# Optimization experiments

Measured on AMD Instinct MI355X. Metric: run time of the kernel, lower is better.

The kernel has to match this reference:

```python
import jax, jax.numpy as jnp
import numpy as np

N = 6144
IN_DIM = 256
HID = 64
HEADS = 4
LAT = 32
ALPHA = 0.2  # LeakyReLU negative slope
NEG_INF = -9e15


def setup_inputs() -> dict:
    key = jax.random.key(0)
    ks = jax.random.split(key, 6)
    x = jax.random.normal(ks[0], (N, IN_DIM), jnp.float32)
    # sparse symmetric 0/1 adjacency, avg degree ~ 25
    A = (jax.random.uniform(ks[1], (N, N)) < 0.004).astype(jnp.float32)
    A = jnp.maximum(A, A.T)
    # xavier-uniform-ish params, matching pyGAT GraphAttentionLayer shapes
    s1 = float(np.sqrt(6.0 / (IN_DIM + HID)))
    W_heads = jax.random.uniform(ks[2], (HEADS, IN_DIM, HID), jnp.float32, -s1, s1)
    sa = float(np.sqrt(6.0 / (2 * HID + 1)))
    a_heads = jax.random.uniform(ks[3], (HEADS, 2 * HID), jnp.float32, -sa, sa)
    s2 = float(np.sqrt(6.0 / (HEADS * HID + LAT)))
    W_out = jax.random.uniform(ks[4], (HEADS * HID, LAT), jnp.float32, -s2, s2)
    sb = float(np.sqrt(6.0 / (2 * LAT + 1)))
    a_out = jax.random.uniform(ks[5], (2 * LAT,), jnp.float32, -sb, sb)
    return {"x": x, "A": A, "W_heads": W_heads, "a_heads": a_heads,
            "W_out": W_out, "a_out": a_out}


def _gat_layer(h, adj_mask, W, a, concat):
    # h: [N, F_in], W: [F_in, F], a: [2F]
    Wh = h @ W                              # [N, F]
    f = W.shape[1]
    e_src = Wh @ a[:f]                      # [N]
    e_dst = Wh @ a[f:]                      # [N]
    e = jax.nn.leaky_relu(e_src[:, None] + e_dst[None, :], ALPHA)  # [N, N]
    e = jnp.where(adj_mask, e, NEG_INF)
    att = jax.nn.softmax(e, axis=1)         # masked softmax over neighbors
    out = att @ Wh                          # [N, F]
    return jax.nn.elu(out) if concat else out


def reference(x, A, W_heads, a_heads, W_out, a_out):
    # normalize(A, 'sym', False): D^{-1/2} A D^{-1/2}
    deg = A.sum(axis=1)
    dinv = jnp.where(deg > 0, deg ** -0.5, 0.0)
    An = A * dinv[:, None] * dinv[None, :]
    mask = An > 0
    heads = [_gat_layer(x, mask, W_heads[i], a_heads[i], True) for i in range(HEADS)]
    h = jnp.concatenate(heads, axis=1)      # [N, HEADS*HID]
    z = jax.nn.elu(_gat_layer(h, mask, W_out, a_out, False))  # [N, LAT]
    return jax.nn.sigmoid(z @ z.T)          # [N, N]
```

## Files before the change

kernel.cpp:

```cpp
#include <hip/hip_runtime.h>
#include <hip/hip_bf16.h>

#define NN 6144
#define IN_DIM 256
#define HID 64
#define HEADS 4
#define LAT 32
#define CAP 192
#define ALPHA 0.2f
#define GEMM_BLOCKS 384

typedef __attribute__((ext_vector_type(8))) short bf16x8;
typedef __attribute__((ext_vector_type(4))) float f32x4;

__device__ __forceinline__ float elu_f(float v)   { return v > 0.f ? v : expm1f(v); }
__device__ __forceinline__ float lrelu_f(float v) { return v > 0.f ? v : ALPHA * v; }

__device__ __forceinline__ void split_bf16(float v, unsigned short& hi, unsigned short& lo) {
    unsigned u = __builtin_bit_cast(unsigned, v);
    hi = (unsigned short)(u >> 16);
    float vh = __builtin_bit_cast(float, u & 0xFFFF0000u);
    float rl = v - vh;
    lo = (unsigned short)(__builtin_bit_cast(unsigned, rl) >> 16);
}

__global__ __launch_bounds__(256) void k_pre(const float* __restrict__ A,
                                             const float* __restrict__ x,
                                             const float* __restrict__ Wheads,
                                             const float* __restrict__ aheads,
                                             int* __restrict__ nbr, int* __restrict__ cnt,
                                             float* __restrict__ Wh,
                                             float* __restrict__ es, float* __restrict__ ed) {
    __shared__ __align__(16) float smem[2048];
    int bid = blockIdx.x;
    int t = threadIdx.x;
    if (bid < GEMM_BLOCKS) {
        int head = bid & 3, m0 = (bid >> 2) * 64;
        float (*As)[64] = (float(*)[64])smem;
        float (*Bs)[64] = (float(*)[64])(smem + 1024);
        const float* Wc = Wheads + (size_t)head * IN_DIM * HID;
        int ty = t >> 4, tx = t & 15;
        float acc[4][4] = {};
        for (int k0 = 0; k0 < IN_DIM; k0 += 16) {
            {
                int row = t >> 2, k4 = (t & 3) * 4;
                float4 v = *(const float4*)(x + (size_t)(m0 + row) * IN_DIM + k0 + k4);
                As[k4 + 0][row] = v.x; As[k4 + 1][row] = v.y;
                As[k4 + 2][row] = v.z; As[k4 + 3][row] = v.w;
                int kk = t >> 4, n4 = (t & 15) * 4;
                *(float4*)&Bs[kk][n4] = *(const float4*)(Wc + (size_t)(k0 + kk) * HID + n4);
            }
            __syncthreads();
            #pragma unroll
            for (int k = 0; k < 16; ++k) {
                float4 av = *(float4*)&As[k][ty * 4];
                float4 bv = *(float4*)&Bs[k][tx * 4];
                float ar[4] = {av.x, av.y, av.z, av.w};
                float br[4] = {bv.x, bv.y, bv.z, bv.w};
                #pragma unroll
                for (int i = 0; i < 4; ++i)
                    #pragma unroll
                    for (int j = 0; j < 4; ++j)
                        acc[i][j] = fmaf(ar[i], br[j], acc[i][j]);
            }
            __syncthreads();
        }
        #pragma unroll
        for (int i = 0; i < 4; ++i) {
            float4 o = make_float4(acc[i][0], acc[i][1], acc[i][2], acc[i][3]);
            *(float4*)(Wh + (size_t)(m0 + ty * 4 + i) * (HEADS * HID) + head * HID + tx * 4) = o;
        }
        float4 a1v = *(const float4*)(aheads + head * 2 * HID + tx * 4);
        float4 a2v = *(const float4*)(aheads + head * 2 * HID + HID + tx * 4);
        #pragma unroll
        for (int i = 0; i < 4; ++i) {
            float p1 = acc[i][0] * a1v.x + acc[i][1] * a1v.y + acc[i][2] * a1v.z + acc[i][3] * a1v.w;
            float p2 = acc[i][0] * a2v.x + acc[i][1] * a2v.y + acc[i][2] * a2v.z + acc[i][3] * a2v.w;
            #pragma unroll
            for (int off = 8; off; off >>= 1) {
                p1 += __shfl_down(p1, off, 16);
                p2 += __shfl_down(p2, off, 16);
            }
            if (tx == 0) {
                es[head * NN + m0 + ty * 4 + i] = p1;
                ed[head * NN + m0 + ty * 4 + i] = p2;
            }
        }
    } else {
        int row = bid - GEMM_BLOCKS;
        int* lcnt = (int*)smem;
        const float4* Arow = (const float4*)(A + (size_t)row * NN);
        if (t == 0) *lcnt = 0;
        __syncthreads();
        int* my = nbr + (size_t)row * CAP;
        #pragma unroll
        for (int it = 0; it < NN / 4 / 256; ++it) {
            int idx4 = it * 256 + t;
            float4 v = Arow[idx4];
            int base = idx4 * 4;
            if (v.x != 0.f) { int p = atomicAdd(lcnt, 1); if (p < CAP) my[p] = base; }
            if (v.y != 0.f) { int p = atomicAdd(lcnt, 1); if (p < CAP) my[p] = base + 1; }
            if (v.z != 0.f) { int p = atomicAdd(lcnt, 1); if (p < CAP) my[p] = base + 2; }
            if (v.w != 0.f) { int p = atomicAdd(lcnt, 1); if (p < CAP) my[p] = base + 3; }
        }
        __syncthreads();
        if (t == 0) cnt[row] = *lcnt < CAP ? *lcnt : CAP;
    }
}

__global__ __launch_bounds__(256, 8) void k_attn1g2(const int* __restrict__ nbr, const int* __restrict__ cnt,
                                                    const float* __restrict__ es, const float* __restrict__ ed,
                                                    const float* __restrict__ Wh,
                                                    const float* __restrict__ Wout, const float* __restrict__ aout,
                                                    float* __restrict__ Wh2,
                                                    float* __restrict__ es2, float* __restrict__ ed2) {
    __shared__ int col[CAP];
    __shared__ float att[HEADS][CAP];
    __shared__ float hrow[HEADS * HID];
    __shared__ float part[8][LAT];
    int i = blockIdx.x;
    int t = threadIdx.x, h = t >> 6, l = t & 63;
    int c = cnt[i];
    float hval;
    if (c == 0) {
        float s = 0.f;
        for (int r = 0; r < NN; ++r) s += Wh[(size_t)r * (HEADS * HID) + h * HID + l];
        hval = elu_f(s * (1.0f / NN));
    } else {
        const int* nb = nbr + (size_t)i * CAP;
        float esi = es[h * NN + i];
        float m = -3.0e38f;
        for (int j = l; j < c; j += 64) {
            int cj = nb[j];
            if (h == 0) col[j] = cj;
            float e = lrelu_f(esi + ed[h * NN + cj]);
            att[h][j] = e;
            m = fmaxf(m, e);
        }
        #pragma unroll
        for (int off = 32; off; off >>= 1) m = fmaxf(m, __shfl_down(m, off));
        m = __shfl(m, 0);
        float s = 0.f;
        for (int j = l; j < c; j += 64) {
            float p = __expf(att[h][j] - m);
            att[h][j] = p;
            s += p;
        }
        #pragma unroll
        for (int off = 32; off; off >>= 1) s += __shfl_down(s, off);
        s = __shfl(s, 0);
        __syncthreads();
        float inv = 1.0f / s;
        const float* WhH = Wh + h * HID + l;
        float a0 = 0.f, a1 = 0.f, a2 = 0.f, a3 = 0.f;
        float a4 = 0.f, a5 = 0.f, a6 = 0.f, a7 = 0.f;
        int j = 0;
        for (; j + 8 <= c; j += 8) {
            a0 = fmaf(att[h][j + 0], WhH[(size_t)col[j + 0] * (HEADS * HID)], a0);
            a1 = fmaf(att[h][j + 1], WhH[(size_t)col[j + 1] * (HEADS * HID)], a1);
            a2 = fmaf(att[h][j + 2], WhH[(size_t)col[j + 2] * (HEADS * HID)], a2);
            a3 = fmaf(att[h][j + 3], WhH[(size_t)col[j + 3] * (HEADS * HID)], a3);
            a4 = fmaf(att[h][j + 4], WhH[(size_t)col[j + 4] * (HEADS * HID)], a4);
            a5 = fmaf(att[h][j + 5], WhH[(size_t)col[j + 5] * (HEADS * HID)], a5);
            a6 = fmaf(att[h][j + 6], WhH[(size_t)col[j + 6] * (HEADS * HID)], a6);
            a7 = fmaf(att[h][j + 7], WhH[(size_t)col[j + 7] * (HEADS * HID)], a7);
        }
        for (; j < c; ++j)
            a0 = fmaf(att[h][j], WhH[(size_t)col[j] * (HEADS * HID)], a0);
        hval = elu_f((((a0 + a1) + (a2 + a3)) + ((a4 + a5) + (a6 + a7))) * inv);
    }
    hrow[h * HID + l] = hval;
    __syncthreads();
    {
        int half = l >> 5, cc = l & 31;
        int tbase = h * HID + half * 32;
        float p = 0.f;
        #pragma unroll 8
        for (int tt = 0; tt < 32; ++tt)
            p = fmaf(hrow[tbase + tt], Wout[(tbase + tt) * LAT + cc], p);
        part[h * 2 + half][cc] = p;
    }
    __syncthreads();
    if (t < 32) {
        float acc = 0.f;
        #pragma unroll
        for (int w = 0; w < 8; ++w) acc += part[w][t];
        Wh2[(size_t)i * LAT + t] = acc;
        float p1 = acc * aout[t], p2 = acc * aout[LAT + t];
        #pragma unroll
        for (int off = 16; off; off >>= 1) {
            p1 += __shfl_down(p1, off, 32);
            p2 += __shfl_down(p2, off, 32);
        }
        if (t == 0) { es2[i] = p1; ed2[i] = p2; }
    }
}

__global__ __launch_bounds__(256, 8) void k_attn2(const int* __restrict__ nbr, const int* __restrict__ cnt,
                                                  const float* __restrict__ es2, const float* __restrict__ ed2,
                                                  const float* __restrict__ Wh2,
                                                  unsigned short* __restrict__ zh, unsigned short* __restrict__ zl) {
    __shared__ float att[4][CAP];
    __shared__ int col[4][CAP];
    int w = threadIdx.x >> 6, l = threadIdx.x & 63;
    int i = blockIdx.x * 4 + w;
    int c = cnt[i];
    if (c == 0) {
        if (l < LAT) {
            float s = 0.f;
            for (int r = 0; r < NN; ++r) s += Wh2[(size_t)r * LAT + l];
            unsigned short hi, lo;
            split_bf16(elu_f(s * (1.0f / NN)), hi, lo);
            zh[(size_t)i * LAT + l] = hi;
            zl[(size_t)i * LAT + l] = lo;
        }
        return;
    }
    float esi = es2[i];
    const int* nb = nbr + (size_t)i * CAP;
    float m = -3.0e38f;
    for (int j = l; j < c; j += 64) {
        int cj = nb[j];
        col[w][j] = cj;
        float e = lrelu_f(esi + ed2[cj]);
        att[w][j] = e;
        m = fmaxf(m, e);
    }
    #pragma unroll
    for (int off = 32; off; off >>= 1) m = fmaxf(m, __shfl_down(m, off));
    m = __shfl(m, 0);
    float s = 0.f;
    for (int j = l; j < c; j += 64) {
        float p = __expf(att[w][j] - m);
        att[w][j] = p;
        s += p;
    }
    #pragma unroll
    for (int off = 32; off; off >>= 1) s += __shfl_down(s, off);
    s = __shfl(s, 0);
    if (l < LAT) {
        float inv = 1.0f / s;
        float a0 = 0.f, a1 = 0.f, a2 = 0.f, a3 = 0.f;
        int j = 0;
        for (; j + 4 <= c; j += 4) {
            a0 = fmaf(att[w][j + 0], Wh2[(size_t)col[w][j + 0] * LAT + l], a0);
            a1 = fmaf(att[w][j + 1], Wh2[(size_t)col[w][j + 1] * LAT + l], a1);
            a2 = fmaf(att[w][j + 2], Wh2[(size_t)col[w][j + 2] * LAT + l], a2);
            a3 = fmaf(att[w][j + 3], Wh2[(size_t)col[w][j + 3] * LAT + l], a3);
        }
        for (; j < c; ++j)
            a0 = fmaf(att[w][j], Wh2[(size_t)col[w][j] * LAT + l], a0);
        unsigned short hi, lo;
        split_bf16(elu_f(((a0 + a1) + (a2 + a3)) * inv), hi, lo);
        zh[(size_t)i * LAT + l] = hi;
        zl[(size_t)i * LAT + l] = lo;
    }
}

__global__ __launch_bounds__(256, 8) void k_zzt(const unsigned short* __restrict__ zh,
                                                const unsigned short* __restrict__ zl,
                                                float* __restrict__ out) {
    int t = threadIdx.x, w = t >> 6, l = t & 63;
    int m0 = blockIdx.y * 64 + w * 16;
    int n0 = blockIdx.x * 64;
    int r = l & 15, kg = (l >> 4) * 8;
    bf16x8 ah = *(const bf16x8*)(zh + (size_t)(m0 + r) * LAT + kg);
    bf16x8 al = *(const bf16x8*)(zl + (size_t)(m0 + r) * LAT + kg);
    #pragma unroll
    for (int jp = 0; jp < 2; ++jp) {
        int nbA = n0 + (jp * 2 + 0) * 16;
        int nbB = n0 + (jp * 2 + 1) * 16;
        bf16x8 bhA = *(const bf16x8*)(zh + (size_t)(nbA + r) * LAT + kg);
        bf16x8 blA = *(const bf16x8*)(zl + (size_t)(nbA + r) * LAT + kg);
        bf16x8 bhB = *(const bf16x8*)(zh + (size_t)(nbB + r) * LAT + kg);
        bf16x8 blB = *(const bf16x8*)(zl + (size_t)(nbB + r) * LAT + kg);
        f32x4 accA = {0.f, 0.f, 0.f, 0.f};
        accA = __builtin_amdgcn_mfma_f32_16x16x32_bf16(ah, bhA, accA, 0, 0, 0);
        accA = __builtin_amdgcn_mfma_f32_16x16x32_bf16(ah, blA, accA, 0, 0, 0);
        accA = __builtin_amdgcn_mfma_f32_16x16x32_bf16(al, bhA, accA, 0, 0, 0);
        f32x4 accB = {0.f, 0.f, 0.f, 0.f};
        accB = __builtin_amdgcn_mfma_f32_16x16x32_bf16(ah, bhB, accB, 0, 0, 0);
        accB = __builtin_amdgcn_mfma_f32_16x16x32_bf16(ah, blB, accB, 0, 0, 0);
        accB = __builtin_amdgcn_mfma_f32_16x16x32_bf16(al, bhB, accB, 0, 0, 0);
        #pragma unroll
        for (int rr = 0; rr < 4; ++rr) {
            int row = m0 + (l >> 4) * 4 + rr;
            out[(size_t)row * NN + nbA + (l & 15)] = 1.0f / (1.0f + __expf(-accA[rr]));
            out[(size_t)row * NN + nbB + (l & 15)] = 1.0f / (1.0f + __expf(-accB[rr]));
        }
    }
}

extern "C" void kernel_launch(void* const* d_in, const int* in_sizes, int n_in,
                              void* d_out, int out_size, void* d_ws, size_t ws_size,
                              hipStream_t stream) {
    const float* x      = (const float*)d_in[0];
    const float* A      = (const float*)d_in[1];
    const float* Wheads = (const float*)d_in[2];
    const float* aheads = (const float*)d_in[3];
    const float* Wout   = (const float*)d_in[4];
    const float* aout   = (const float*)d_in[5];
    float* out = (float*)d_out;

    char* ws = (char*)d_ws;
    size_t o = 0;
    auto alloc = [&](size_t bytes) { void* p = ws + o; o += (bytes + 255) & ~(size_t)255; return p; };
    int*   nbr   = (int*)  alloc((size_t)NN * CAP * 4);
    int*   cnt   = (int*)  alloc((size_t)NN * 4);
    float* Wh    = (float*)alloc((size_t)NN * HEADS * HID * 4);
    float* es    = (float*)alloc((size_t)HEADS * NN * 4);
    float* ed    = (float*)alloc((size_t)HEADS * NN * 4);
    float* Wh2   = (float*)alloc((size_t)NN * LAT * 4);
    float* es2   = (float*)alloc((size_t)NN * 4);
    float* ed2   = (float*)alloc((size_t)NN * 4);
    unsigned short* zh = (unsigned short*)alloc((size_t)NN * LAT * 2);
    unsigned short* zl = (unsigned short*)alloc((size_t)NN * LAT * 2);

    k_pre     <<<GEMM_BLOCKS + NN, 256, 0, stream>>>(A, x, Wheads, aheads, nbr, cnt, Wh, es, ed);
    k_attn1g2 <<<NN, 256, 0, stream>>>(nbr, cnt, es, ed, Wh, Wout, aout, Wh2, es2, ed2);
    k_attn2   <<<NN / 4, 256, 0, stream>>>(nbr, cnt, es2, ed2, Wh2, zh, zl);
    k_zzt     <<<dim3(NN / 64, NN / 64), 256, 0, stream>>>(zh, zl, out);
}
```

Measured before the change: 115.6 us.

## Fuse adjacency scan into attention kernel and vectorize sigmoid output stores

Splits the former combined GEMM+adjacency-scan kernel into a standalone GEMM, and moves the per-row adjacency scan into the first attention kernel, which builds neighbor lists directly in shared memory and skips re-reading them from global memory. It also changes the ZZ^T output write to store float4s along the transposed index, relying on symmetry of the output. This is meant to cut a global round trip for neighbor lists and make output stores wider. The trade-off is that the attention kernel now serializes the dense A row scan before compute.

```diff
diff --git a/kernel.cpp b/kernel.cpp
--- a/kernel.cpp
+++ b/kernel.cpp
@@ -8,7 +8,6 @@
 #define LAT 32
 #define CAP 192
 #define ALPHA 0.2f
-#define GEMM_BLOCKS 384
 
 typedef __attribute__((ext_vector_type(8))) short bf16x8;
 typedef __attribute__((ext_vector_type(4))) float f32x4;
@@ -24,116 +23,108 @@
     lo = (unsigned short)(__builtin_bit_cast(unsigned, rl) >> 16);
 }
 
-__global__ __launch_bounds__(256) void k_pre(const float* __restrict__ A,
-                                             const float* __restrict__ x,
-                                             const float* __restrict__ Wheads,
-                                             const float* __restrict__ aheads,
-                                             int* __restrict__ nbr, int* __restrict__ cnt,
-                                             float* __restrict__ Wh,
-                                             float* __restrict__ es, float* __restrict__ ed) {
-    __shared__ __align__(16) float smem[2048];
-    int bid = blockIdx.x;
+__global__ __launch_bounds__(256) void k_gemm1(const float* __restrict__ x,
+                                               const float* __restrict__ Wheads,
+                                               const float* __restrict__ aheads,
+                                               float* __restrict__ Wh,
+                                               float* __restrict__ es, float* __restrict__ ed) {
+    __shared__ float As[16][64];
+    __shared__ float Bs[16][64];
+    int head = blockIdx.x & 3, m0 = (blockIdx.x >> 2) * 64;
+    const float* Wc = Wheads + (size_t)head * IN_DIM * HID;
     int t = threadIdx.x;
-    if (bid < GEMM_BLOCKS) {
-        int head = bid & 3, m0 = (bid >> 2) * 64;
-        float (*As)[64] = (float(*)[64])smem;
-        float (*Bs)[64] = (float(*)[64])(smem + 1024);
-        const float* Wc = Wheads + (size_t)head * IN_DIM * HID;
-        int ty = t >> 4, tx = t & 15;
-        float acc[4][4] = {};
-        for (int k0 = 0; k0 < IN_DIM; k0 += 16) {
-            {
-                int row = t >> 2, k4 = (t & 3) * 4;
-                float4 v = *(const float4*)(x + (size_t)(m0 + row) * IN_DIM + k0 + k4);
-                As[k4 + 0][row] = v.x; As[k4 + 1][row] = v.y;
-                As[k4 + 2][row] = v.z; As[k4 + 3][row] = v.w;
-                int kk = t >> 4, n4 = (t & 15) * 4;
-                *(float4*)&Bs[kk][n4] = *(const float4*)(Wc + (size_t)(k0 + kk) * HID + n4);
-            }
-            __syncthreads();
+    int ty = t >> 4, tx = t & 15;
+    float acc[4][4] = {};
+    for (int k0 = 0; k0 < IN_DIM; k0 += 16) {
+        {
+            int row = t >> 2, k4 = (t & 3) * 4;
+            float4 v = *(const float4*)(x + (size_t)(m0 + row) * IN_DIM + k0 + k4);
+            As[k4 + 0][row] = v.x; As[k4 + 1][row] = v.y;
+            As[k4 + 2][row] = v.z; As[k4 + 3][row] = v.w;
+            int kk = t >> 4, n4 = (t & 15) * 4;
+            *(float4*)&Bs[kk][n4] = *(const float4*)(Wc + (size_t)(k0 + kk) * HID + n4);
+        }
+        __syncthreads();
+        #pragma unroll
+        for (int k = 0; k < 16; ++k) {
+            float4 av = *(float4*)&As[k][ty * 4];
+            float4 bv = *(float4*)&Bs[k][tx * 4];
+            float ar[4] = {av.x, av.y, av.z, av.w};
+            float br[4] = {bv.x, bv.y, bv.z, bv.w};
             #pragma unroll
-            for (int k = 0; k < 16; ++k) {
-                float4 av = *(float4*)&As[k][ty * 4];
-                float4 bv = *(float4*)&Bs[k][tx * 4];
-                float ar[4] = {av.x, av.y, av.z, av.w};
-                float br[4] = {bv.x, bv.y, bv.z, bv.w};
+            for (int i = 0; i < 4; ++i)
                 #pragma unroll
-                for (int i = 0; i < 4; ++i)
-                    #pragma unroll
-                    for (int j = 0; j < 4; ++j)
-                        acc[i][j] = fmaf(ar[i], br[j], acc[i][j]);
-            }
-            __syncthreads();
-        }
-        #pragma unroll
-        for (int i = 0; i < 4; ++i) {
-            float4 o = make_float4(acc[i][0], acc[i][1], acc[i][2], acc[i][3]);
-            *(float4*)(Wh + (size_t)(m0 + ty * 4 + i) * (HEADS * HID) + head * HID + tx * 4) = o;
-        }
-        float4 a1v = *(const float4*)(aheads + head * 2 * HID + tx * 4);
-        float4 a2v = *(const float4*)(aheads + head * 2 * HID + HID + tx * 4);
-        #pragma unroll
-        for (int i = 0; i < 4; ++i) {
-            float p1 = acc[i][0] * a1v.x + acc[i][1] * a1v.y + acc[i][2] * a1v.z + acc[i][3] * a1v.w;
-            float p2 = acc[i][0] * a2v.x + acc[i][1] * a2v.y + acc[i][2] * a2v.z + acc[i][3] * a2v.w;
-            #pragma unroll
-            for (int off = 8; off; off >>= 1) {
-                p1 += __shfl_down(p1, off, 16);
-                p2 += __shfl_down(p2, off, 16);
-            }
-            if (tx == 0) {
-                es[head * NN + m0 + ty * 4 + i] = p1;
-                ed[head * NN + m0 + ty * 4 + i] = p2;
-            }
-        }
-    } else {
-        int row = bid - GEMM_BLOCKS;
-        int* lcnt = (int*)smem;
-        const float4* Arow = (const float4*)(A + (size_t)row * NN);
-        if (t == 0) *lcnt = 0;
+                for (int j = 0; j < 4; ++j)
+                    acc[i][j] = fmaf(ar[i], br[j], acc[i][j]);
+        }
         __syncthreads();
-        int* my = nbr + (size_t)row * CAP;
-        #pragma unroll
-        for (int it = 0; it < NN / 4 / 256; ++it) {
-            int idx4 = it * 256 + t;
-            float4 v = Arow[idx4];
-            int base = idx4 * 4;
-            if (v.x != 0.f) { int p = atomicAdd(lcnt, 1); if (p < CAP) my[p] = base; }
-            if (v.y != 0.f) { int p = atomicAdd(lcnt, 1); if (p < CAP) my[p] = base + 1; }
-            if (v.z != 0.f) { int p = atomicAdd(lcnt, 1); if (p < CAP) my[p] = base + 2; }
-            if (v.w != 0.f) { int p = atomicAdd(lcnt, 1); if (p < CAP) my[p] = base + 3; }
-        }
-        __syncthreads();
-        if (t == 0) cnt[row] = *lcnt < CAP ? *lcnt : CAP;
-    }
-}
-
-__global__ __launch_bounds__(256, 8) void k_attn1g2(const int* __restrict__ nbr, const int* __restrict__ cnt,
+    }
+    #pragma unroll
+    for (int i = 0; i < 4; ++i) {
+        float4 o = make_float4(acc[i][0], acc[i][1], acc[i][2], acc[i][3]);
+        *(float4*)(Wh + (size_t)(m0 + ty * 4 + i) * (HEADS * HID) + head * HID + tx * 4) = o;
+    }
+    float4 a1v = *(const float4*)(aheads + head * 2 * HID + tx * 4);
+    float4 a2v = *(const float4*)(aheads + head * 2 * HID + HID + tx * 4);
+    #pragma unroll
+    for (int i = 0; i < 4; ++i) {
+        float p1 = acc[i][0] * a1v.x + acc[i][1] * a1v.y + acc[i][2] * a1v.z + acc[i][3] * a1v.w;
+        float p2 = acc[i][0] * a2v.x + acc[i][1] * a2v.y + acc[i][2] * a2v.z + acc[i][3] * a2v.w;
+        #pragma unroll
+        for (int off = 8; off; off >>= 1) {
+            p1 += __shfl_down(p1, off, 16);
+            p2 += __shfl_down(p2, off, 16);
+        }
+        if (tx == 0) {
+            es[head * NN + m0 + ty * 4 + i] = p1;
+            ed[head * NN + m0 + ty * 4 + i] = p2;
+        }
+    }
+}
+
+__global__ __launch_bounds__(256, 8) void k_rowattn(const float* __restrict__ A,
+                                                    int* __restrict__ nbr, int* __restrict__ cnt,
                                                     const float* __restrict__ es, const float* __restrict__ ed,
                                                     const float* __restrict__ Wh,
                                                     const float* __restrict__ Wout, const float* __restrict__ aout,
                                                     float* __restrict__ Wh2,
                                                     float* __restrict__ es2, float* __restrict__ ed2) {
-    __shared__ int col[CAP];
+    __shared__ int colS[CAP];
     __shared__ float att[HEADS][CAP];
     __shared__ float hrow[HEADS * HID];
     __shared__ float part[8][LAT];
+    __shared__ int lcnt;
     int i = blockIdx.x;
     int t = threadIdx.x, h = t >> 6, l = t & 63;
-    int c = cnt[i];
+
+    if (t == 0) lcnt = 0;
+    __syncthreads();
+    const float4* Arow = (const float4*)(A + (size_t)i * NN);
+    #pragma unroll
+    for (int it = 0; it < NN / 4 / 256; ++it) {
+        int idx4 = it * 256 + t;
+        float4 v = Arow[idx4];
+        int base = idx4 * 4;
+        if (v.x != 0.f) { int p = atomicAdd(&lcnt, 1); if (p < CAP) colS[p] = base; }
+        if (v.y != 0.f) { int p = atomicAdd(&lcnt, 1); if (p < CAP) colS[p] = base + 1; }
+        if (v.z != 0.f) { int p = atomicAdd(&lcnt, 1); if (p < CAP) colS[p] = base + 2; }
+        if (v.w != 0.f) { int p = atomicAdd(&lcnt, 1); if (p < CAP) colS[p] = base + 3; }
+    }
+    __syncthreads();
+    int c = lcnt < CAP ? lcnt : CAP;
+    if (t == 0) cnt[i] = c;
+    for (int j = t; j < c; j += 256) nbr[(size_t)i * CAP + j] = colS[j];
+
     float hval;
     if (c == 0) {
         float s = 0.f;
         for (int r = 0; r < NN; ++r) s += Wh[(size_t)r * (HEADS * HID) + h * HID + l];
         hval = elu_f(s * (1.0f / NN));
     } else {
-        const int* nb = nbr + (size_t)i * CAP;
         float esi = es[h * NN + i];
         float m = -3.0e38f;
         for (int j = l; j < c; j += 64) {
-            int cj = nb[j];
-            if (h == 0) col[j] = cj;
-            float e = lrelu_f(esi + ed[h * NN + cj]);
+            float e = lrelu_f(esi + ed[h * NN + colS[j]]);
             att[h][j] = e;
             m = fmaxf(m, e);
         }
@@ -156,17 +147,17 @@
         float a4 = 0.f, a5 = 0.f, a6 = 0.f, a7 = 0.f;
         int j = 0;
         for (; j + 8 <= c; j += 8) {
-            a0 = fmaf(att[h][j + 0], WhH[(size_t)col[j + 0] * (HEADS * HID)], a0);
-            a1 = fmaf(att[h][j + 1], WhH[(size_t)col[j + 1] * (HEADS * HID)], a1);
-            a2 = fmaf(att[h][j + 2], WhH[(size_t)col[j + 2] * (HEADS * HID)], a2);
-            a3 = fmaf(att[h][j + 3], WhH[(size_t)col[j + 3] * (HEADS * HID)], a3);
-            a4 = fmaf(att[h][j + 4], WhH[(size_t)col[j + 4] * (HEADS * HID)], a4);
-            a5 = fmaf(att[h][j + 5], WhH[(size_t)col[j + 5] * (HEADS * HID)], a5);
-            a6 = fmaf(att[h][j + 6], WhH[(size_t)col[j + 6] * (HEADS * HID)], a6);
-            a7 = fmaf(att[h][j + 7], WhH[(size_t)col[j + 7] * (HEADS * HID)], a7);
+            a0 = fmaf(att[h][j + 0], WhH[(size_t)colS[j + 0] * (HEADS * HID)], a0);
+            a1 = fmaf(att[h][j + 1], WhH[(size_t)colS[j + 1] * (HEADS * HID)], a1);
+            a2 = fmaf(att[h][j + 2], WhH[(size_t)colS[j + 2] * (HEADS * HID)], a2);
+            a3 = fmaf(att[h][j + 3], WhH[(size_t)colS[j + 3] * (HEADS * HID)], a3);
+            a4 = fmaf(att[h][j + 4], WhH[(size_t)colS[j + 4] * (HEADS * HID)], a4);
+            a5 = fmaf(att[h][j + 5], WhH[(size_t)colS[j + 5] * (HEADS * HID)], a5);
+            a6 = fmaf(att[h][j + 6], WhH[(size_t)colS[j + 6] * (HEADS * HID)], a6);
+            a7 = fmaf(att[h][j + 7], WhH[(size_t)colS[j + 7] * (HEADS * HID)], a7);
         }
         for (; j < c; ++j)
-            a0 = fmaf(att[h][j], WhH[(size_t)col[j] * (HEADS * HID)], a0);
+            a0 = fmaf(att[h][j], WhH[(size_t)colS[j] * (HEADS * HID)], a0);
         hval = elu_f((((a0 + a1) + (a2 + a3)) + ((a4 + a5) + (a6 + a7))) * inv);
     }
     hrow[h * HID + l] = hval;
@@ -266,6 +257,7 @@
     int r = l & 15, kg = (l >> 4) * 8;
     bf16x8 ah = *(const bf16x8*)(zh + (size_t)(m0 + r) * LAT + kg);
     bf16x8 al = *(const bf16x8*)(zl + (size_t)(m0 + r) * LAT + kg);
+    int mbase = m0 + (l >> 4) * 4;
     #pragma unroll
     for (int jp = 0; jp < 2; ++jp) {
         int nbA = n0 + (jp * 2 + 0) * 16;
@@ -282,12 +274,17 @@
         accB = __builtin_amdgcn_mfma_f32_16x16x32_bf16(ah, bhB, accB, 0, 0, 0);
         accB = __builtin_amdgcn_mfma_f32_16x16x32_bf16(ah, blB, accB, 0, 0, 0);
         accB = __builtin_amdgcn_mfma_f32_16x16x32_bf16(al, bhB, accB, 0, 0, 0);
-        #pragma unroll
-        for (int rr = 0; rr < 4; ++rr) {
-            int row = m0 + (l >> 4) * 4 + rr;
-            out[(size_t)row * NN + nbA + (l & 15)] = 1.0f / (1.0f + __expf(-accA[rr]));
-            out[(size_t)row * NN + nbB + (l & 15)] = 1.0f / (1.0f + __expf(-accB[rr]));
-        }
+        float4 oA, oB;
+        oA.x = 1.0f / (1.0f + __expf(-accA[0]));
+        oA.y = 1.0f / (1.0f + __expf(-accA[1]));
+        oA.z = 1.0f / (1.0f + __expf(-accA[2]));
+        oA.w = 1.0f / (1.0f + __expf(-accA[3]));
+        oB.x = 1.0f / (1.0f + __expf(-accB[0]));
+        oB.y = 1.0f / (1.0f + __expf(-accB[1]));
+        oB.z = 1.0f / (1.0f + __expf(-accB[2]));
+        oB.w = 1.0f / (1.0f + __expf(-accB[3]));
+        *(float4*)(out + (size_t)(nbA + (l & 15)) * NN + mbase) = oA;
+        *(float4*)(out + (size_t)(nbB + (l & 15)) * NN + mbase) = oB;
     }
 }
 
@@ -316,8 +313,8 @@
     unsigned short* zh = (unsigned short*)alloc((size_t)NN * LAT * 2);
     unsigned short* zl = (unsigned short*)alloc((size_t)NN * LAT * 2);
 
-    k_pre     <<<GEMM_BLOCKS + NN, 256, 0, stream>>>(A, x, Wheads, aheads, nbr, cnt, Wh, es, ed);
-    k_attn1g2 <<<NN, 256, 0, stream>>>(nbr, cnt, es, ed, Wh, Wout, aout, Wh2, es2, ed2);
+    k_gemm1   <<<(NN / 64) * HEADS, 256, 0, stream>>>(x, Wheads, aheads, Wh, es, ed);
+    k_rowattn <<<NN, 256, 0, stream>>>(A, nbr, cnt, es, ed, Wh, Wout, aout, Wh2, es2, ed2);
     k_attn2   <<<NN / 4, 256, 0, stream>>>(nbr, cnt, es2, ed2, Wh2, zh, zl);
     k_zzt     <<<dim3(NN / 64, NN / 64), 256, 0, stream>>>(zh, zl, out);
 }
```

After: 132.5 us. 1.15x slower.
